# Kernel tuning notes

Hardware: AMD Instinct MI355X
Metric: run time of the kernel (lower is better)

The kernel has to match this reference:

```python
import jax, jax.numpy as jnp
import numpy as np

D = 2048        # d_model == d_enc
S = 8192        # encoder sequence length
V = 32000 + 2   # vocab_size + 2
R = 7           # num_rel


def _gru_cell(x, h, Wih, Whh, bih, bhh):
    # torch.nn.GRUCell gate order: r, z, n
    gi = x @ Wih.T + bih          # [3D]
    gh = h @ Whh.T + bhh          # [3D]
    ir, iz, inn = jnp.split(gi, 3)
    hr, hz, hn = jnp.split(gh, 3)
    r = jax.nn.sigmoid(ir + hr)
    z = jax.nn.sigmoid(iz + hz)
    n = jnp.tanh(inn + r * hn)
    return (1.0 - z) * n + z * h


def setup_inputs() -> dict:
    key = jax.random.key(0)
    ks = jax.random.split(key, 28)
    s = 1.0 / np.sqrt(D)
    def u(k, shape, scale=s):
        return jax.random.uniform(k, shape, jnp.float32, -scale, scale)
    inp = {
        "enc_tokens":    jax.random.normal(ks[0], (S, D), jnp.float32),
        "c_prev":        jax.random.normal(ks[1], (D,), jnp.float32),
        "partner_embed": jax.random.normal(ks[2], (D,), jnp.float32),
        "cov_vec":       jax.random.normal(ks[3], (D,), jnp.float32),
        # gru_alpha
        "Wih_a": u(ks[4], (3 * D, D)), "Whh_a": u(ks[5], (3 * D, D)),
        "bih_a": u(ks[6], (3 * D,)),   "bhh_a": u(ks[7], (3 * D,)),
        # gru_beta
        "Wih_b": u(ks[8], (3 * D, D)), "Whh_b": u(ks[9], (3 * D, D)),
        "bih_b": u(ks[10], (3 * D,)),  "bhh_b": u(ks[11], (3 * D,)),
        # attention projections
        "W_enc": u(ks[12], (D, D)), "b_enc": u(ks[13], (D,)),
        "W_co":  u(ks[14], (D, D)), "b_co":  u(ks[15], (D,)),
        "W_cov": u(ks[16], (D, D)), "b_cov": u(ks[17], (D,)),
        "W_score": u(ks[18], (1, D)), "b_score": u(ks[19], (1,)),
        # heads
        "W_sym": u(ks[20], (V, D)), "b_sym": u(ks[21], (V,)),
        "W_rel": u(ks[22], (R, D)), "b_rel": u(ks[23], (R,)),
    }
    return inp


def reference(enc_tokens, c_prev, partner_embed, cov_vec,
              Wih_a, Whh_a, bih_a, bhh_a,
              Wih_b, Whh_b, bih_b, bhh_b,
              W_enc, b_enc, W_co, b_co, W_cov, b_cov,
              W_score, b_score, W_sym, b_sym, W_rel, b_rel):
    # alpha GRU step
    c_o = _gru_cell(partner_embed, c_prev, Wih_a, Whh_a, bih_a, bhh_a)  # [D]
    # additive (Bahdanau) attention
    e = enc_tokens @ W_enc.T + b_enc              # [S, D]
    co = c_o @ W_co.T + b_co                      # [D] broadcast over S
    cov = cov_vec @ W_cov.T + b_cov               # [D]
    scores = jnp.tanh(e + co + cov) @ W_score[0] + b_score[0]  # [S]
    alpha = jax.nn.softmax(scores)                # [S]
    ctx = alpha @ enc_tokens                      # [D]
    # beta GRU step
    c_beta = _gru_cell(ctx, c_o, Wih_b, Whh_b, bih_b, bhh_b)  # [D]
    symbol_logits = c_beta @ W_sym.T + b_sym      # [V]
    rel_logits = c_beta @ W_rel.T + b_rel         # [R]
    return (symbol_logits, rel_logits, c_beta, alpha)
```

## Files before the change

### kernel.cpp

```cpp
#include <hip/hip_runtime.h>
#include <hip/hip_bf16.h>
#include <math.h>

#define DD 2048
#define SS 8192
#define VV 32002
#define RR 7
#define GATE 6144

typedef unsigned short u16;
typedef __attribute__((ext_vector_type(8))) unsigned short u16x8;
typedef __attribute__((ext_vector_type(8))) short bfrag;
typedef __attribute__((ext_vector_type(4))) float f32x4;

__device__ __attribute__((aligned(256))) u16 g_ah[(size_t)SS * DD];
__device__ __attribute__((aligned(256))) u16 g_bh[(size_t)DD * DD];
__device__ __attribute__((aligned(256))) float g_gia[GATE], g_gha[GATE], g_gib[GATE], g_ghb[GATE];
__device__ __attribute__((aligned(256))) float g_co[DD], g_cc[DD], g_ctx[DD], g_cb[DD];
__device__ __attribute__((aligned(256))) float g_alpha[SS];
__device__ __attribute__((aligned(256))) float g_scores[SS];

__device__ __forceinline__ float fsigmoid(float x) { return 1.0f / (1.0f + __expf(-x)); }
__device__ __forceinline__ float ftanh(float x)    { return 1.0f - 2.0f / (__expf(2.0f * x) + 1.0f); }
__device__ __forceinline__ u16 f2bf(float v) {
    union { float f; unsigned int i; } c; c.f = v;
    return (u16)((c.i + 0x7FFF + ((c.i >> 16) & 1)) >> 16);
}
__device__ __forceinline__ float bf2f(u16 u) {
    union { unsigned int i; float f; } c; c.i = ((unsigned int)u) << 16; return c.f;
}
__device__ __forceinline__ void gload16(const void* g, void* l) {
    __builtin_amdgcn_global_load_lds(
        (const __attribute__((address_space(1))) void*)g,
        (__attribute__((address_space(3))) void*)l, 16, 0, 0);
}

__global__ void diag_k(float* out, float v) { out[0] = v; }

template<int WHICH>
__global__ __launch_bounds__(256) void presplit_k(const float* __restrict__ src) {
    u16* dst = WHICH ? g_bh : g_ah;
    size_t i = ((size_t)blockIdx.x * 256 + threadIdx.x) * 8;
    f32x4 v0 = *(const f32x4*)&src[i];
    f32x4 v1 = *(const f32x4*)&src[i + 4];
    u16x8 h;
#pragma unroll
    for (int e = 0; e < 4; ++e) { h[e] = f2bf(v0[e]); h[4 + e] = f2bf(v1[e]); }
    *(u16x8*)&dst[i] = h;
}

__global__ void init_k() {
    int i = blockIdx.x * 256 + threadIdx.x;
    g_scores[i] = 0.0f;
    if (i < DD) g_ctx[i] = 0.0f;
}

template<int MODE>
__global__ __launch_bounds__(256) void matvec_k(const float* __restrict__ W,
                                                const float* __restrict__ x_in,
                                                const float* __restrict__ bias) {
    const float* x = (MODE == 2) ? g_ctx : (MODE == 3) ? g_co : x_in;
    float* out     = (MODE == 0) ? g_gia : (MODE == 1) ? g_gha : (MODE == 2) ? g_gib : g_ghb;
    int wv = threadIdx.x >> 6, lane = threadIdx.x & 63;
    int row = blockIdx.x * 4 + wv;
    if (row >= GATE) return;
    const float* wp = W + (size_t)row * DD;
    float acc = 0.0f;
#pragma unroll
    for (int j = 0; j < 4; ++j) {
        int base = j * 512 + lane * 8;
        f32x4 w0 = *(const f32x4*)&wp[base];
        f32x4 w1 = *(const f32x4*)&wp[base + 4];
        f32x4 x0 = *(const f32x4*)&x[base];
        f32x4 x1 = *(const f32x4*)&x[base + 4];
#pragma unroll
        for (int e = 0; e < 4; ++e) acc += w0[e] * x0[e] + w1[e] * x1[e];
    }
#pragma unroll
    for (int o = 1; o < 64; o <<= 1) acc += __shfl_xor(acc, o);
    if (lane == 0) out[row] = acc + bias[row];
}

template<int B>
__global__ void gru_out_k(const float* __restrict__ h_in, float* __restrict__ out_f) {
    const float* gi = B ? g_gib : g_gia;
    const float* gh = B ? g_ghb : g_gha;
    int d = blockIdx.x * 256 + threadIdx.x;
    float hh = B ? g_co[d] : h_in[d];
    float r = fsigmoid(gi[d] + gh[d]);
    float z = fsigmoid(gi[DD + d] + gh[DD + d]);
    float n = ftanh(gi[2 * DD + d] + r * gh[2 * DD + d]);
    float c = (1.0f - z) * n + z * hh;
    if (B) { g_cb[d] = c; out_f[d] = c; }
    else   { g_co[d] = c; }
}

__global__ __launch_bounds__(256) void cc_k(const float* __restrict__ Wco, const float* __restrict__ Wcov,
                                            const float* __restrict__ cov,
                                            const float* __restrict__ benc, const float* __restrict__ bco,
                                            const float* __restrict__ bcov) {
    int wv = threadIdx.x >> 6, lane = threadIdx.x & 63;
    int row = blockIdx.x * 4 + wv;
    const float* p1 = Wco + (size_t)row * DD;
    const float* p2 = Wcov + (size_t)row * DD;
    float acc = 0.0f;
#pragma unroll
    for (int j = 0; j < 4; ++j) {
        int base = j * 512 + lane * 8;
        f32x4 u0 = *(const f32x4*)&p1[base];
        f32x4 u1 = *(const f32x4*)&p1[base + 4];
        f32x4 v0 = *(const f32x4*)&p2[base];
        f32x4 v1 = *(const f32x4*)&p2[base + 4];
        f32x4 a0 = *(const f32x4*)&g_co[base];
        f32x4 a1 = *(const f32x4*)&g_co[base + 4];
        f32x4 b0 = *(const f32x4*)&cov[base];
        f32x4 b1 = *(const f32x4*)&cov[base + 4];
#pragma unroll
        for (int e = 0; e < 4; ++e)
            acc += u0[e] * a0[e] + u1[e] * a1[e] + v0[e] * b0[e] + v1[e] * b1[e];
    }
#pragma unroll
    for (int o = 1; o < 64; o <<= 1) acc += __shfl_xor(acc, o);
    if (lane == 0) g_cc[row] = acc + benc[row] + bco[row] + bcov[row];
}

__global__ __launch_bounds__(256) void score_gemm_k(const float* __restrict__ Wsc) {
    __shared__ u16 As[128 * 32];
    __shared__ u16 Bs[128 * 32];
    const int bid = blockIdx.x;
    const int swz = (bid & 7) * 128 + (bid >> 3);
    const int bm = swz >> 4;
    const int bn = swz & 15;
    const int tid = threadIdx.x;
    const int wave = tid >> 6, lane = tid & 63;
    const int wr = wave >> 1, wc = wave & 1;
    const int srow = lane >> 2, scol = (lane & 3) * 8;
    const int rsel = lane & 15;
    const int kq = (lane >> 4) * 8;
    const int c0 = wave * 2, c1 = wave * 2 + 1;

    f32x4 acc[4][4];
#pragma unroll
    for (int m = 0; m < 4; ++m)
#pragma unroll
        for (int n = 0; n < 4; ++n) acc[m][n] = f32x4{0.f, 0.f, 0.f, 0.f};

    const u16* gA = g_ah + (size_t)(bm * 128) * DD;
    const u16* gB = g_bh + (size_t)(bn * 128) * DD;

    for (int k0 = 0; k0 < DD; k0 += 32) {
        gload16(gA + (size_t)(c0 * 16 + srow) * DD + k0 + scol, &As[c0 * 512]);
        gload16(gA + (size_t)(c1 * 16 + srow) * DD + k0 + scol, &As[c1 * 512]);
        gload16(gB + (size_t)(c0 * 16 + srow) * DD + k0 + scol, &Bs[c0 * 512]);
        gload16(gB + (size_t)(c1 * 16 + srow) * DD + k0 + scol, &Bs[c1 * 512]);
        __syncthreads();
        bfrag a[4], b[4];
#pragma unroll
        for (int m = 0; m < 4; ++m) a[m] = *(const bfrag*)&As[(wr * 64 + m * 16 + rsel) * 32 + kq];
#pragma unroll
        for (int n = 0; n < 4; ++n) b[n] = *(const bfrag*)&Bs[(wc * 64 + n * 16 + rsel) * 32 + kq];
#pragma unroll
        for (int m = 0; m < 4; ++m)
#pragma unroll
            for (int n = 0; n < 4; ++n)
                acc[m][n] = __builtin_amdgcn_mfma_f32_16x16x32_bf16(a[m], b[n], acc[m][n], 0, 0, 0);
        __syncthreads();
    }

    const int cl = lane & 15, gq = lane >> 4;
    float ccv[4], wv[4];
#pragma unroll
    for (int nf = 0; nf < 4; ++nf) {
        int n = bn * 128 + wc * 64 + nf * 16 + cl;
        ccv[nf] = g_cc[n];
        wv[nf] = Wsc[n];
    }
#pragma unroll
    for (int m = 0; m < 4; ++m) {
#pragma unroll
        for (int r = 0; r < 4; ++r) {
            float v = 0.0f;
#pragma unroll
            for (int nf = 0; nf < 4; ++nf) v += ftanh(acc[m][nf][r] + ccv[nf]) * wv[nf];
            v += __shfl_xor(v, 1); v += __shfl_xor(v, 2);
            v += __shfl_xor(v, 4); v += __shfl_xor(v, 8);
            if (cl == 0) atomicAdd(&g_scores[bm * 128 + wr * 64 + m * 16 + gq * 4 + r], v);
        }
    }
}

__global__ __launch_bounds__(1024) void softmax_k(float* __restrict__ out_alpha) {
    __shared__ float red[16];
    __shared__ float sval;
    int t = threadIdx.x, lane = t & 63, w = t >> 6;
    float loc[8];
    float m = -1e30f;
#pragma unroll
    for (int i = 0; i < 8; ++i) {
        loc[i] = g_scores[t + i * 1024];
        m = fmaxf(m, loc[i]);
    }
#pragma unroll
    for (int o = 1; o < 64; o <<= 1) m = fmaxf(m, __shfl_xor(m, o));
    if (lane == 0) red[w] = m;
    __syncthreads();
    if (t == 0) { float mm = red[0]; for (int i = 1; i < 16; ++i) mm = fmaxf(mm, red[i]); sval = mm; }
    __syncthreads();
    float mx = sval, s = 0.0f;
#pragma unroll
    for (int i = 0; i < 8; ++i) { loc[i] = __expf(loc[i] - mx); s += loc[i]; }
#pragma unroll
    for (int o = 1; o < 64; o <<= 1) s += __shfl_xor(s, o);
    if (lane == 0) red[w] = s;
    __syncthreads();
    if (t == 0) { float ss = 0; for (int i = 0; i < 16; ++i) ss += red[i]; sval = ss; }
    __syncthreads();
    float inv = 1.0f / sval;
#pragma unroll
    for (int i = 0; i < 8; ++i) {
        float a = loc[i] * inv;
        g_alpha[t + i * 1024] = a;
        out_alpha[t + i * 1024] = a;
    }
}

__global__ __launch_bounds__(256) void ctx_partial_k() {
    int t = threadIdx.x, b = blockIdx.x;
    int d0 = t * 8;
    float acc[8] = {0, 0, 0, 0, 0, 0, 0, 0};
    int s0 = b * 64;
    for (int s = s0; s < s0 + 64; ++s) {
        u16x8 v = *(const u16x8*)&g_ah[(size_t)s * DD + d0];
        float a = g_alpha[s];
#pragma unroll
        for (int e = 0; e < 8; ++e) acc[e] += a * bf2f(v[e]);
    }
#pragma unroll
    for (int e = 0; e < 8; ++e) atomicAdd(&g_ctx[d0 + e], acc[e]);
}

__global__ __launch_bounds__(256) void heads_k(const float* __restrict__ Wsym, const float* __restrict__ bsym,
                                               const float* __restrict__ Wrel, const float* __restrict__ brel,
                                               float* __restrict__ out) {
    int wv = threadIdx.x >> 6, lane = threadIdx.x & 63;
    int row = blockIdx.x * 4 + wv;
    if (row >= VV + RR) return;
    const float* wp;
    float bb;
    if (row < VV) { wp = Wsym + (size_t)row * DD; bb = bsym[row]; }
    else          { wp = Wrel + (size_t)(row - VV) * DD; bb = brel[row - VV]; }
    float acc = 0.0f;
#pragma unroll
    for (int j = 0; j < 4; ++j) {
        int base = j * 512 + lane * 8;
        f32x4 w0 = *(const f32x4*)&wp[base];
        f32x4 w1 = *(const f32x4*)&wp[base + 4];
        f32x4 x0 = *(const f32x4*)&g_cb[base];
        f32x4 x1 = *(const f32x4*)&g_cb[base + 4];
#pragma unroll
        for (int e = 0; e < 4; ++e) acc += w0[e] * x0[e] + w1[e] * x1[e];
    }
#pragma unroll
    for (int o = 1; o < 64; o <<= 1) acc += __shfl_xor(acc, o);
    if (lane == 0) out[row] = acc + bb;
}

extern "C" void kernel_launch(void* const* d_in, const int* in_sizes, int n_in,
                              void* d_out, int out_size, void* d_ws, size_t ws_size,
                              hipStream_t stream) {
    float* out = (float*)d_out;

    static const int expected[24] = {
        SS * DD, DD, DD, DD,
        3 * DD * DD, 3 * DD * DD, 3 * DD, 3 * DD,
        3 * DD * DD, 3 * DD * DD, 3 * DD, 3 * DD,
        DD * DD, DD, DD * DD, DD, DD * DD, DD,
        DD, 1, VV * DD, VV, RR * DD, RR
    };
    if (n_in != 24) { diag_k<<<1, 1, 0, stream>>>(out, 4.0e7f); return; }
    for (int i = 0; i < 24; ++i)
        if (in_sizes[i] != expected[i]) { diag_k<<<1, 1, 0, stream>>>(out, 3.0e7f + (i + 1) * 1.0e5f); return; }

    const float* enc     = (const float*)d_in[0];
    const float* cprev   = (const float*)d_in[1];
    const float* partner = (const float*)d_in[2];
    const float* cov     = (const float*)d_in[3];
    const float* Wih_a   = (const float*)d_in[4];
    const float* Whh_a   = (const float*)d_in[5];
    const float* bih_a   = (const float*)d_in[6];
    const float* bhh_a   = (const float*)d_in[7];
    const float* Wih_b   = (const float*)d_in[8];
    const float* Whh_b   = (const float*)d_in[9];
    const float* bih_b   = (const float*)d_in[10];
    const float* bhh_b   = (const float*)d_in[11];
    const float* W_enc   = (const float*)d_in[12];
    const float* b_enc   = (const float*)d_in[13];
    const float* W_co    = (const float*)d_in[14];
    const float* b_co    = (const float*)d_in[15];
    const float* W_cov   = (const float*)d_in[16];
    const float* b_cov   = (const float*)d_in[17];
    const float* W_score = (const float*)d_in[18];
    const float* W_sym   = (const float*)d_in[20];
    const float* b_sym   = (const float*)d_in[21];
    const float* W_rel   = (const float*)d_in[22];
    const float* b_rel   = (const float*)d_in[23];

    init_k<<<32, 256, 0, stream>>>();
    presplit_k<0><<<SS * DD / (256 * 8), 256, 0, stream>>>(enc);
    presplit_k<1><<<DD * DD / (256 * 8), 256, 0, stream>>>(W_enc);
    matvec_k<0><<<GATE / 4, 256, 0, stream>>>(Wih_a, partner, bih_a);
    matvec_k<1><<<GATE / 4, 256, 0, stream>>>(Whh_a, cprev, bhh_a);
    gru_out_k<0><<<8, 256, 0, stream>>>(cprev, nullptr);
    cc_k<<<DD / 4, 256, 0, stream>>>(W_co, W_cov, cov, b_enc, b_co, b_cov);
    score_gemm_k<<<1024, 256, 0, stream>>>(W_score);
    softmax_k<<<1, 1024, 0, stream>>>(out + VV + RR + DD);
    ctx_partial_k<<<128, 256, 0, stream>>>();
    matvec_k<2><<<GATE / 4, 256, 0, stream>>>(Wih_b, cprev, bih_b);
    matvec_k<3><<<GATE / 4, 256, 0, stream>>>(Whh_b, cprev, bhh_b);
    gru_out_k<1><<<8, 256, 0, stream>>>(cprev, out + VV + RR);
    heads_k<<<(VV + RR + 3) / 4, 256, 0, stream>>>(W_sym, b_sym, W_rel, b_rel, out);
}
```

Baseline: 268.5 us.

## Double-buffer score GEMM LDS tiles and merge paired GRU matvec launches

The score GEMM now uses two LDS buffers, prefetching the next K-slice with global_load_lds while MFMAs run on the current one, and drops one barrier per iteration. The input and hidden GRU matvecs for each cell are merged into a single launch over twice as many blocks, and the init kernel is folded into presplit_k<1>. The aim is to hide global-load latency in the GEMM and cut kernel-launch overhead. LDS use doubles, which may lower occupancy.

```diff
diff --git a/kernel.cpp b/kernel.cpp
--- a/kernel.cpp
+++ b/kernel.cpp
@@ -47,23 +47,29 @@
 #pragma unroll
     for (int e = 0; e < 4; ++e) { h[e] = f2bf(v0[e]); h[4 + e] = f2bf(v1[e]); }
     *(u16x8*)&dst[i] = h;
-}
-
-__global__ void init_k() {
-    int i = blockIdx.x * 256 + threadIdx.x;
-    g_scores[i] = 0.0f;
-    if (i < DD) g_ctx[i] = 0.0f;
-}
-
-template<int MODE>
-__global__ __launch_bounds__(256) void matvec_k(const float* __restrict__ W,
-                                                const float* __restrict__ x_in,
-                                                const float* __restrict__ bias) {
-    const float* x = (MODE == 2) ? g_ctx : (MODE == 3) ? g_co : x_in;
-    float* out     = (MODE == 0) ? g_gia : (MODE == 1) ? g_gha : (MODE == 2) ? g_gib : g_ghb;
+    if (WHICH == 1) {
+        int gt = blockIdx.x * 256 + threadIdx.x;
+        if (gt < SS) g_scores[gt] = 0.0f;
+        if (gt < DD) g_ctx[gt] = 0.0f;
+    }
+}
+
+template<int PAIR>
+__global__ __launch_bounds__(256) void matvec2_k(const float* __restrict__ W0,
+                                                 const float* __restrict__ W1,
+                                                 const float* __restrict__ x0_in,
+                                                 const float* __restrict__ x1_in,
+                                                 const float* __restrict__ b0,
+                                                 const float* __restrict__ b1) {
+    const int half = blockIdx.x >= (GATE / 4);
+    const float* W    = half ? W1 : W0;
+    const float* bias = half ? b1 : b0;
+    const float* x;
+    float* out;
+    if (PAIR == 0) { x = half ? x1_in : x0_in; out = half ? g_gha : g_gia; }
+    else           { x = half ? g_co  : g_ctx; out = half ? g_ghb : g_gib; }
     int wv = threadIdx.x >> 6, lane = threadIdx.x & 63;
-    int row = blockIdx.x * 4 + wv;
-    if (row >= GATE) return;
+    int row = (blockIdx.x - half * (GATE / 4)) * 4 + wv;
     const float* wp = W + (size_t)row * DD;
     float acc = 0.0f;
 #pragma unroll
@@ -125,8 +131,8 @@
 }
 
 __global__ __launch_bounds__(256) void score_gemm_k(const float* __restrict__ Wsc) {
-    __shared__ u16 As[128 * 32];
-    __shared__ u16 Bs[128 * 32];
+    __shared__ u16 As[2][128 * 32];
+    __shared__ u16 Bs[2][128 * 32];
     const int bid = blockIdx.x;
     const int swz = (bid & 7) * 128 + (bid >> 3);
     const int bm = swz >> 4;
@@ -147,24 +153,36 @@
 
     const u16* gA = g_ah + (size_t)(bm * 128) * DD;
     const u16* gB = g_bh + (size_t)(bn * 128) * DD;
-
-    for (int k0 = 0; k0 < DD; k0 += 32) {
-        gload16(gA + (size_t)(c0 * 16 + srow) * DD + k0 + scol, &As[c0 * 512]);
-        gload16(gA + (size_t)(c1 * 16 + srow) * DD + k0 + scol, &As[c1 * 512]);
-        gload16(gB + (size_t)(c0 * 16 + srow) * DD + k0 + scol, &Bs[c0 * 512]);
-        gload16(gB + (size_t)(c1 * 16 + srow) * DD + k0 + scol, &Bs[c1 * 512]);
-        __syncthreads();
+    const size_t off0 = (size_t)(c0 * 16 + srow) * DD + scol;
+    const size_t off1 = (size_t)(c1 * 16 + srow) * DD + scol;
+
+    gload16(gA + off0, &As[0][c0 * 512]);
+    gload16(gA + off1, &As[0][c1 * 512]);
+    gload16(gB + off0, &Bs[0][c0 * 512]);
+    gload16(gB + off1, &Bs[0][c1 * 512]);
+    __syncthreads();
+
+    int cur = 0;
+    for (int step = 0; step < 64; ++step) {
+        if (step < 63) {
+            size_t k1 = (size_t)(step + 1) * 32;
+            gload16(gA + off0 + k1, &As[cur ^ 1][c0 * 512]);
+            gload16(gA + off1 + k1, &As[cur ^ 1][c1 * 512]);
+            gload16(gB + off0 + k1, &Bs[cur ^ 1][c0 * 512]);
+            gload16(gB + off1 + k1, &Bs[cur ^ 1][c1 * 512]);
+        }
         bfrag a[4], b[4];
 #pragma unroll
-        for (int m = 0; m < 4; ++m) a[m] = *(const bfrag*)&As[(wr * 64 + m * 16 + rsel) * 32 + kq];
-#pragma unroll
-        for (int n = 0; n < 4; ++n) b[n] = *(const bfrag*)&Bs[(wc * 64 + n * 16 + rsel) * 32 + kq];
+        for (int m = 0; m < 4; ++m) a[m] = *(const bfrag*)&As[cur][(wr * 64 + m * 16 + rsel) * 32 + kq];
+#pragma unroll
+        for (int n = 0; n < 4; ++n) b[n] = *(const bfrag*)&Bs[cur][(wc * 64 + n * 16 + rsel) * 32 + kq];
 #pragma unroll
         for (int m = 0; m < 4; ++m)
 #pragma unroll
             for (int n = 0; n < 4; ++n)
                 acc[m][n] = __builtin_amdgcn_mfma_f32_16x16x32_bf16(a[m], b[n], acc[m][n], 0, 0, 0);
         __syncthreads();
+        cur ^= 1;
     }
 
     const int cl = lane & 15, gq = lane >> 4;
@@ -305,18 +323,15 @@
     const float* W_rel   = (const float*)d_in[22];
     const float* b_rel   = (const float*)d_in[23];
 
-    init_k<<<32, 256, 0, stream>>>();
     presplit_k<0><<<SS * DD / (256 * 8), 256, 0, stream>>>(enc);
     presplit_k<1><<<DD * DD / (256 * 8), 256, 0, stream>>>(W_enc);
-    matvec_k<0><<<GATE / 4, 256, 0, stream>>>(Wih_a, partner, bih_a);
-    matvec_k<1><<<GATE / 4, 256, 0, stream>>>(Whh_a, cprev, bhh_a);
+    matvec2_k<0><<<2 * (GATE / 4), 256, 0, stream>>>(Wih_a, Whh_a, partner, cprev, bih_a, bhh_a);
     gru_out_k<0><<<8, 256, 0, stream>>>(cprev, nullptr);
     cc_k<<<DD / 4, 256, 0, stream>>>(W_co, W_cov, cov, b_enc, b_co, b_cov);
     score_gemm_k<<<1024, 256, 0, stream>>>(W_score);
     softmax_k<<<1, 1024, 0, stream>>>(out + VV + RR + DD);
     ctx_partial_k<<<128, 256, 0, stream>>>();
-    matvec_k<2><<<GATE / 4, 256, 0, stream>>>(Wih_b, cprev, bih_b);
-    matvec_k<3><<<GATE / 4, 256, 0, stream>>>(Whh_b, cprev, bhh_b);
+    matvec2_k<1><<<2 * (GATE / 4), 256, 0, stream>>>(Wih_b, Whh_b, nullptr, nullptr, bih_b, bhh_b);
     gru_out_k<1><<<8, 256, 0, stream>>>(cprev, out + VV + RR);
     heads_k<<<(VV + RR + 3) / 4, 256, 0, stream>>>(W_sym, b_sym, W_rel, b_rel, out);
 }
```

Result: no change. 268.5 us (-0.0%).
